# Optimization experiments

Measured on AMD Instinct MI355X. Metric: run time of the kernel, lower is better.

The kernel has to match this reference:

```python
import jax, jax.numpy as jnp
import numpy as np

B, S, D, R, N = 4, 2048, 1024, 256, 16

def setup_inputs() -> dict:
    key = jax.random.key(0)
    k1, k2, k3, k4, k5 = jax.random.split(key, 5)
    return {
        "x": jax.random.normal(k1, (B, S, D), dtype=jnp.float32),
        "feature_know": jax.random.normal(k2, (N, D, R), dtype=jnp.float32) * 0.02,
        "restore_know": jax.random.normal(k3, (N, R, D), dtype=jnp.float32) * 0.02,
        "feature_know_w": jax.random.uniform(k4, (B, S, N), dtype=jnp.float32),
        "restore_know_w": jax.random.uniform(k5, (B, S, N), dtype=jnp.float32),
    }

def reference(x, feature_know, restore_know, feature_know_w, restore_know_w):
    # Feature stage: weighted mixture over N knowledge neurons, D -> R.
    # Same math as einsum('bsd,ndr->bsnr') then einsum('bsnr,bsn->bsr'),
    # fused so the [B,S,N,R] intermediate is reduced over N on the fly.
    h = jnp.einsum('bsd,ndr,bsn->bsr', x, feature_know, feature_know_w)
    # Restore stage: R -> D, again a weighted mixture over N neurons.
    out = jnp.einsum('bsr,nrd,bsn->bsd', h, restore_know, restore_know_w)
    # Dropout is evaluated deterministically (eval mode): identity.
    return out
```

## Files before the change

kernel.cpp:

```cpp
#include <hip/hip_runtime.h>

typedef unsigned short u16;
typedef unsigned int u32;
typedef __attribute__((ext_vector_type(4))) float f32x4;
typedef __attribute__((ext_vector_type(8))) short bf16x8;
typedef __attribute__((ext_vector_type(4))) unsigned short u16x4;

#define MFMA(a, b, c) __builtin_amdgcn_mfma_f32_16x16x32_bf16((a), (b), (c), 0, 0, 0)

static constexpr int M_TOK = 8192;

__device__ __forceinline__ u16 f2bf(float f) {
  u32 u = __float_as_uint(f);
  return (u16)((u + 0x7FFFu + ((u >> 16) & 1u)) >> 16);
}
__device__ __forceinline__ float bf2f(u16 b) {
  u32 u = ((u32)b) << 16;
  return __uint_as_float(u);
}
__device__ __forceinline__ void gload16(const u16* g, u16* l) {
  __builtin_amdgcn_global_load_lds(
      (const __attribute__((address_space(1))) u32*)(const void*)g,
      (__attribute__((address_space(3))) u32*)(void*)l, 16, 0, 0);
}

#define PH_BAR()                                       \
  do {                                                 \
    __builtin_amdgcn_s_barrier();                      \
    asm volatile("s_waitcnt lgkmcnt(0)" ::: "memory"); \
  } while (0)
#define PH_END() __builtin_amdgcn_s_barrier()

__global__ void cast_x_kernel(const float* __restrict__ in, u16* __restrict__ out, int total4) {
  for (int i = blockIdx.x * blockDim.x + threadIdx.x; i < total4; i += gridDim.x * blockDim.x) {
    float4 v = ((const float4*)in)[i];
    u16x4 o;
    o[0] = f2bf(v.x); o[1] = f2bf(v.y); o[2] = f2bf(v.z); o[3] = f2bf(v.w);
    ((u16x4*)out)[i] = o;
  }
}

__global__ void tcast_kernel(const float* __restrict__ in, u16* __restrict__ out, int P, int Q) {
  __shared__ float tile[32][33];
  const int z = blockIdx.z;
  const int q0 = blockIdx.x * 32, p0 = blockIdx.y * 32;
  const float* src = in + (size_t)z * P * Q;
  u16* dst = out + (size_t)z * P * Q;
  const int tx = threadIdx.x & 31, ty = threadIdx.x >> 5;
#pragma unroll
  for (int k = 0; k < 4; ++k)
    tile[ty + k * 8][tx] = src[(size_t)(p0 + ty + k * 8) * Q + q0 + tx];
  __syncthreads();
#pragma unroll
  for (int k = 0; k < 4; ++k)
    dst[(size_t)(q0 + ty + k * 8) * P + p0 + tx] = f2bf(tile[tx][ty + k * 8]);
}

__global__ void combine_h(const u16* __restrict__ T, const float* __restrict__ Wf,
                          u16* __restrict__ h) {
  const int m = blockIdx.x * 4 + (threadIdx.x >> 6);
  const int lane = threadIdx.x & 63;
  const u16* rowp = T + (size_t)m * 4096;
  float h0 = 0.f, h1 = 0.f, h2 = 0.f, h3 = 0.f;
#pragma unroll
  for (int n = 0; n < 16; ++n) {
    u16x4 v = *(const u16x4*)&rowp[n * 256 + lane * 4];
    const float wf = Wf[(size_t)m * 16 + n];
    h0 += wf * bf2f(v[0]); h1 += wf * bf2f(v[1]);
    h2 += wf * bf2f(v[2]); h3 += wf * bf2f(v[3]);
  }
  u16x4 o;
  o[0] = f2bf(h0); o[1] = f2bf(h1); o[2] = f2bf(h2); o[3] = f2bf(h3);
  *(u16x4*)&h[(size_t)m * 256 + lane * 4] = o;
}

template <int NT>
__global__ __launch_bounds__(512, 2) void gemm256(
    const u16* __restrict__ A, const u16* __restrict__ Bm, void* __restrict__ OutV,
    const int N, const int K) {
  constexpr int NITER = NT / 2;
  __shared__ u16 lds[65536];

  const int tid = threadIdx.x;
  const int lane = tid & 63;
  const int wid = tid >> 6;
  const int wr = wid >> 2, wc = wid & 3;

  const int L = blockIdx.y * gridDim.x + blockIdx.x;
  const int ordered = (L & 7) * 64 + (L >> 3);
  const int cid = ordered >> 5, win = ordered & 31;
  const int bx = (cid & 3) * 4 + (win & 3);
  const int by = (cid >> 2) * 8 + (win >> 2);
  const int m0 = by * 256, bn0 = bx * 256;

  const int arow = lane & 15;
  const int acol = (lane >> 4) * 16;
  const int sw = (arow & 7) << 4;
  const int lo0 = arow * 128 + (acol ^ sw);
  const int lo1 = arow * 128 + ((64 + acol) ^ sw);

  const u16* Abase = A + (size_t)m0 * K;
  const u16* Bbase = Bm + (size_t)bn0 * K;

  f32x4 acc[8][4];
#pragma unroll
  for (int i = 0; i < 8; ++i)
#pragma unroll
    for (int j = 0; j < 4; ++j) acc[i][j] = (f32x4){0.f, 0.f, 0.f, 0.f};

  auto STAGE = [&](int b, int isB, int hf, int kt) {
    const u16* G = isB ? Bbase : Abase;
    u16* Lp = &lds[isB * 32768 + (b * 2 + hf) * 8192];
#pragma unroll
    for (int j = 0; j < 2; ++j) {
      const int q = j * 8192 + tid * 16;
      const int grow = q >> 7;
      const int gcol = ((q & 127) ^ (((q >> 7) & 7) << 4)) >> 1;
      gload16(G + (size_t)(hf * 128 + grow) * K + kt * 64 + gcol,
              Lp + ((j * 8192 + wid * 1024) >> 1));
    }
  };
  auto LOAD_AV = [&](bf16x8 (&v)[4][2], int b, int mh) {
    const char* p = (const char*)lds + b * 32768 + (wr * 128 + mh * 64) * 128;
#pragma unroll
    for (int mi = 0; mi < 4; ++mi) {
      v[mi][0] = *(const bf16x8*)(p + mi * 2048 + lo0);
      v[mi][1] = *(const bf16x8*)(p + mi * 2048 + lo1);
    }
  };
  auto LOAD_BV = [&](bf16x8 (&v)[2][2], int b, int nq) {
#pragma unroll
    for (int nj = 0; nj < 2; ++nj) {
      const int rb = wc * 64 + (nq * 2 + nj) * 16;
      const char* p = (const char*)lds + 65536 + b * 32768 + rb * 128;
      v[nj][0] = *(const bf16x8*)(p + lo0);
      v[nj][1] = *(const bf16x8*)(p + lo1);
    }
  };

#define QUAD2(AV, BV0, BV1, MH)                                                \
  do {                                                                         \
    _Pragma("unroll") for (int ks = 0; ks < 2; ++ks) {                         \
      _Pragma("unroll") for (int mi = 0; mi < 4; ++mi) {                       \
        _Pragma("unroll") for (int nj = 0; nj < 2; ++nj) {                     \
          acc[(MH)*4 + mi][nj] = MFMA(AV[mi][ks], BV0[nj][ks], acc[(MH)*4 + mi][nj]); \
          acc[(MH)*4 + mi][2 + nj] = MFMA(AV[mi][ks], BV1[nj][ks], acc[(MH)*4 + mi][2 + nj]); \
        }                                                                      \
      }                                                                        \
    }                                                                          \
  } while (0)

  bf16x8 av[4][2], avh[4][2], bv0[2][2], bv1[2][2];

  STAGE(0, 0, 0, 0); STAGE(0, 0, 1, 0); STAGE(0, 1, 0, 0); STAGE(0, 1, 1, 0);
  STAGE(1, 1, 0, 1); STAGE(1, 0, 0, 1);
  asm volatile("s_waitcnt vmcnt(4)" ::: "memory");
  __builtin_amdgcn_s_barrier();

#pragma unroll 1
  for (int i = 0; i < NITER; ++i) {
    const int ta = 2 * i, tb = ta + 1;
    const bool st = (i + 1 < NITER);
    LOAD_AV(av, 0, 0); LOAD_BV(bv0, 0, 0); LOAD_BV(bv1, 0, 1);
    STAGE(1, 0, 1, tb); STAGE(1, 1, 1, tb);
    PH_BAR();
    __builtin_amdgcn_s_setprio(1);
    QUAD2(av, bv0, bv1, 0);
    __builtin_amdgcn_s_setprio(0);
    PH_END();
    LOAD_AV(avh, 0, 1);
    if (st) { STAGE(0, 1, 0, ta + 2); STAGE(0, 0, 0, ta + 2); }
    PH_BAR();
    __builtin_amdgcn_s_setprio(1);
    QUAD2(avh, bv0, bv1, 1);
    __builtin_amdgcn_s_setprio(0);
    if (st) asm volatile("s_waitcnt vmcnt(4)" ::: "memory");
    else    asm volatile("s_waitcnt vmcnt(0)" ::: "memory");
    PH_END();
    LOAD_AV(av, 1, 0); LOAD_BV(bv0, 1, 0); LOAD_BV(bv1, 1, 1);
    if (st) { STAGE(0, 0, 1, ta + 2); STAGE(0, 1, 1, ta + 2); }
    PH_BAR();
    __builtin_amdgcn_s_setprio(1);
    QUAD2(av, bv0, bv1, 0);
    __builtin_amdgcn_s_setprio(0);
    PH_END();
    LOAD_AV(avh, 1, 1);
    if (st) { STAGE(1, 1, 0, tb + 2); STAGE(1, 0, 0, tb + 2); }
    PH_BAR();
    __builtin_amdgcn_s_setprio(1);
    QUAD2(avh, bv0, bv1, 1);
    __builtin_amdgcn_s_setprio(0);
    if (st) asm volatile("s_waitcnt vmcnt(4)" ::: "memory");
    PH_END();
  }

#pragma unroll
  for (int MI = 0; MI < 8; ++MI) {
    const int r0 = wr * 128 + MI * 16 + (lane >> 4) * 4;
#pragma unroll
    for (int NJ = 0; NJ < 4; ++NJ) {
      const int c = wc * 64 + NJ * 16 + (lane & 15);
#pragma unroll
      for (int j = 0; j < 4; ++j) {
        const int rr = r0 + j;
        *(u16*)((char*)lds + ((rr * 512 + c * 2) ^ ((rr & 7) << 4))) = f2bf(acc[MI][NJ][j]);
      }
    }
  }
  __syncthreads();
#pragma unroll
  for (int i = 0; i < 16; ++i) {
    const int rr = wid * 32 + i * 2 + (lane >> 5);
    const int unit = lane & 31;
    bf16x8 v = *(const bf16x8*)((const char*)lds + ((rr * 512 + unit * 16) ^ ((rr & 7) << 4)));
    *(bf16x8*)((u16*)OutV + (size_t)(m0 + rr) * N + bn0 + unit * 8) = v;
  }
}
#undef QUAD2

__global__ __launch_bounds__(512, 2) void gemm_fold(
    const u16* __restrict__ A,
    const u16* __restrict__ Bn,
    const float* __restrict__ W,
    float* __restrict__ Out) {
  __shared__ u16 ldsB[8][8192];
  __shared__ u16 Wlds[16][264];

  const int tid = threadIdx.x;
  const int lane = tid & 63;
  const int wid = tid >> 6;
  const int kh = wid >> 2;
  const int wrM = (wid >> 1) & 1;
  const int wcN = wid & 1;

  const int L = blockIdx.y * gridDim.x + blockIdx.x;
  const int ordered = (L & 7) * 64 + (L >> 3);
  const int cid = ordered >> 5, win = ordered & 31;
  const int bx = (cid & 3) * 2 + (win & 1);
  const int by = (cid >> 2) * 16 + (win >> 1);
  const int m0 = by * 128, d0 = bx * 128;

  const int arow = lane & 15;
  const int acol = (lane >> 4) * 16;
  const int sw = (arow & 7) << 4;
  const int lo0 = arow * 128 + (acol ^ sw);
  const int lo1 = arow * 128 + ((64 + acol) ^ sw);

  for (int i = tid; i < 128 * 16; i += 512) {
    const int row = i >> 4, n = i & 15;
    Wlds[n][row] = f2bf(W[(size_t)(m0 + row) * 16 + n]);
  }

  auto ASTAGE = [&](int kt) {
    const u16* G = A + (size_t)m0 * 256;
    u16* Lp = &ldsB[kt][0];
#pragma unroll
    for (int j = 0; j < 2; ++j) {
      const int q = j * 8192 + tid * 16;
      const int grow = q >> 7;
      const int gcol = ((q & 127) ^ (((q >> 7) & 7) << 4)) >> 1;
      gload16(G + (size_t)grow * 256 + kt * 64 + gcol, Lp + ((j * 8192 + wid * 1024) >> 1));
    }
  };
  ASTAGE(0); ASTAGE(1); ASTAGE(2); ASTAGE(3);
  __syncthreads();
  bf16x8 avk[4][4];
#pragma unroll
  for (int c2 = 0; c2 < 2; ++c2) {
#pragma unroll
    for (int mi = 0; mi < 4; ++mi) {
      const char* p = (const char*)&ldsB[kh * 2 + c2][0] + (wrM * 64 + mi * 16) * 128;
      avk[c2 * 2 + 0][mi] = *(const bf16x8*)(p + lo0);
      avk[c2 * 2 + 1][mi] = *(const bf16x8*)(p + lo1);
    }
  }
  __syncthreads();

  auto BSTAGE = [&](int ss) {
    const int n = ss >> 1, h = ss & 1, p = ss & 3;
    const u16* G = Bn + ((size_t)n * 1024 + d0) * 256;
#pragma unroll
    for (int t = 0; t < 2; ++t) {
      u16* Lp = &ldsB[2 * p + t][0];
      const int kt = h + 2 * t;
#pragma unroll
      for (int j = 0; j < 2; ++j) {
        const int q = j * 8192 + tid * 16;
        const int grow = q >> 7;
        const int gcol = ((q & 127) ^ (((q >> 7) & 7) << 4)) >> 1;
        gload16(G + (size_t)grow * 256 + kt * 64 + gcol, Lp + ((j * 8192 + wid * 1024) >> 1));
      }
    }
  };

  f32x4 acc_t[4][4], acc_g[4][4];
#pragma unroll
  for (int mi = 0; mi < 4; ++mi)
#pragma unroll
    for (int nj = 0; nj < 4; ++nj) {
      acc_t[mi][nj] = (f32x4){0.f, 0.f, 0.f, 0.f};
      acc_g[mi][nj] = (f32x4){0.f, 0.f, 0.f, 0.f};
    }
  bf16x8 bv[4][2];

  BSTAGE(0); BSTAGE(1); BSTAGE(2);
  asm volatile("s_waitcnt vmcnt(8)" ::: "memory");
  __builtin_amdgcn_s_barrier();

  auto SSTEP = [&](int ss, int h, bool do_stage, int vmsel) {
    const int p = ss & 3;
    const char* pB = (const char*)&ldsB[2 * p + kh][0];
#pragma unroll
    for (int nj = 0; nj < 4; ++nj) {
      const char* q = pB + (wcN * 64 + nj * 16) * 128;
      bv[nj][0] = *(const bf16x8*)(q + lo0);
      bv[nj][1] = *(const bf16x8*)(q + lo1);
    }
    if (do_stage) BSTAGE(ss + 3);
    PH_BAR();
    __builtin_amdgcn_s_setprio(1);
#pragma unroll
    for (int ks = 0; ks < 2; ++ks)
#pragma unroll
      for (int mi = 0; mi < 4; ++mi)
#pragma unroll
        for (int nj = 0; nj < 4; ++nj)
          acc_g[mi][nj] = MFMA(avk[2 * h + ks][mi], bv[nj][ks], acc_g[mi][nj]);
    __builtin_amdgcn_s_setprio(0);
    if (vmsel == 8)      asm volatile("s_waitcnt vmcnt(8)" ::: "memory");
    else if (vmsel == 4) asm volatile("s_waitcnt vmcnt(4)" ::: "memory");
    else if (vmsel == 0) asm volatile("s_waitcnt vmcnt(0)" ::: "memory");
    PH_END();
  };
  auto FOLD = [&](int n) {
#pragma unroll
    for (int mi = 0; mi < 4; ++mi) {
      const int rbase = wrM * 64 + mi * 16 + (lane >> 4) * 4;
      u16x4 wq = *(const u16x4*)&Wlds[n][rbase];
      const float w0 = bf2f(wq[0]), w1 = bf2f(wq[1]), w2 = bf2f(wq[2]), w3 = bf2f(wq[3]);
#pragma unroll
      for (int nj = 0; nj < 4; ++nj) {
        acc_t[mi][nj][0] += w0 * acc_g[mi][nj][0];
        acc_t[mi][nj][1] += w1 * acc_g[mi][nj][1];
        acc_t[mi][nj][2] += w2 * acc_g[mi][nj][2];
        acc_t[mi][nj][3] += w3 * acc_g[mi][nj][3];
        acc_g[mi][nj] = (f32x4){0.f, 0.f, 0.f, 0.f};
      }
    }
  };

#pragma unroll 1
  for (int nn = 0; nn < 14; ++nn) {
    SSTEP(nn * 2 + 0, 0, true, 8);
    SSTEP(nn * 2 + 1, 1, true, 8);
    FOLD(nn);
  }
  SSTEP(28, 0, true, 8);
  SSTEP(29, 1, false, 4);
  FOLD(14);
  SSTEP(30, 0, false, 0);
  SSTEP(31, 1, false, -1);
  FOLD(15);

  __syncthreads();
  float* red = (float*)&ldsB[0][0];
  const int reg = (wrM * 2 + wcN) * 4096;
  if (kh == 1) {
#pragma unroll
    for (int mi = 0; mi < 4; ++mi)
#pragma unroll
      for (int j = 0; j < 4; ++j) {
        const int r = mi * 16 + (lane >> 4) * 4 + j;
#pragma unroll
        for (int nj = 0; nj < 4; ++nj)
          red[reg + r * 64 + nj * 16 + (lane & 15)] = acc_t[mi][nj][j];
      }
  }
  __syncthreads();
  if (kh == 0) {
#pragma unroll
    for (int mi = 0; mi < 4; ++mi) {
      const int rr = mi * 16 + (lane >> 4) * 4;
#pragma unroll
      for (int j = 0; j < 4; ++j) {
        float* orow = Out + (size_t)(m0 + wrM * 64 + rr + j) * 1024 + d0 + wcN * 64 + (lane & 15);
#pragma unroll
        for (int nj = 0; nj < 4; ++nj)
          orow[nj * 16] = acc_t[mi][nj][j] + red[reg + (rr + j) * 64 + nj * 16 + (lane & 15)];
      }
    }
  }
}

extern "C" void kernel_launch(void* const* d_in, const int* in_sizes, int n_in,
                              void* d_out, int out_size, void* d_ws, size_t ws_size,
                              hipStream_t stream) {
  const float* x  = (const float*)d_in[0];
  const float* F  = (const float*)d_in[1];
  const float* Rk = (const float*)d_in[2];
  const float* Wf = (const float*)d_in[3];
  const float* Wr = (const float*)d_in[4];
  float* out = (float*)d_out;

  char* ws = (char*)d_ws;
  u16* X16 = (u16*)(ws);
  u16* B1  = (u16*)(ws + (16u << 20));
  u16* Rt  = (u16*)(ws + (24u << 20));
  u16* T   = (u16*)(ws + (32u << 20));
  u16* h16 = (u16*)(ws);

  cast_x_kernel<<<2048, 256, 0, stream>>>(x, X16, (M_TOK * 1024) / 4);
  tcast_kernel<<<dim3(8, 32, 16), 256, 0, stream>>>(F, B1, 1024, 256);
  tcast_kernel<<<dim3(32, 8, 16), 256, 0, stream>>>(Rk, Rt, 256, 1024);

  gemm256<16><<<dim3(16, 32, 1), 512, 0, stream>>>(X16, B1, T, 4096, 1024);
  combine_h<<<2048, 256, 0, stream>>>(T, Wf, h16);
  gemm_fold<<<dim3(8, 64, 1), 512, 0, stream>>>(h16, Rt, Wr, out);
}
```

Measured before the change: 169.6 us.

## Fuse feature-weight combine into first GEMM epilogue, dropping T intermediate

```diff
diff --git a/kernel.cpp b/kernel.cpp
--- a/kernel.cpp
+++ b/kernel.cpp
@@ -56,30 +56,12 @@
     dst[(size_t)(q0 + ty + k * 8) * P + p0 + tx] = f2bf(tile[tx][ty + k * 8]);
 }
 
-__global__ void combine_h(const u16* __restrict__ T, const float* __restrict__ Wf,
-                          u16* __restrict__ h) {
-  const int m = blockIdx.x * 4 + (threadIdx.x >> 6);
-  const int lane = threadIdx.x & 63;
-  const u16* rowp = T + (size_t)m * 4096;
-  float h0 = 0.f, h1 = 0.f, h2 = 0.f, h3 = 0.f;
-#pragma unroll
-  for (int n = 0; n < 16; ++n) {
-    u16x4 v = *(const u16x4*)&rowp[n * 256 + lane * 4];
-    const float wf = Wf[(size_t)m * 16 + n];
-    h0 += wf * bf2f(v[0]); h1 += wf * bf2f(v[1]);
-    h2 += wf * bf2f(v[2]); h3 += wf * bf2f(v[3]);
-  }
-  u16x4 o;
-  o[0] = f2bf(h0); o[1] = f2bf(h1); o[2] = f2bf(h2); o[3] = f2bf(h3);
-  *(u16x4*)&h[(size_t)m * 256 + lane * 4] = o;
-}
-
-template <int NT>
-__global__ __launch_bounds__(512, 2) void gemm256(
-    const u16* __restrict__ A, const u16* __restrict__ Bm, void* __restrict__ OutV,
-    const int N, const int K) {
-  constexpr int NITER = NT / 2;
+__global__ __launch_bounds__(512, 2) void gemm_h(
+    const u16* __restrict__ A, const u16* __restrict__ Bm,
+    const float* __restrict__ Wf, u16* __restrict__ Hout, const int K) {
+  constexpr int NITER = 8;
   __shared__ u16 lds[65536];
+  __shared__ float wf_lds[256 * 16];
 
   const int tid = threadIdx.x;
   const int lane = tid & 63;
@@ -91,7 +73,7 @@
   const int cid = ordered >> 5, win = ordered & 31;
   const int bx = (cid & 3) * 4 + (win & 3);
   const int by = (cid >> 2) * 8 + (win >> 2);
-  const int m0 = by * 256, bn0 = bx * 256;
+  const int m0 = by * 256, bx16 = bx * 16;
 
   const int arow = lane & 15;
   const int acol = (lane >> 4) * 16;
@@ -100,7 +82,12 @@
   const int lo1 = arow * 128 + ((64 + acol) ^ sw);
 
   const u16* Abase = A + (size_t)m0 * K;
-  const u16* Bbase = Bm + (size_t)bn0 * K;
+
+#pragma unroll
+  for (int t = 0; t < 2; ++t) {
+    const int i4 = t * 512 + tid;
+    *(float4*)&wf_lds[i4 * 4] = *(const float4*)&Wf[(size_t)m0 * 16 + i4 * 4];
+  }
 
   f32x4 acc[8][4];
 #pragma unroll
@@ -109,15 +96,16 @@
     for (int j = 0; j < 4; ++j) acc[i][j] = (f32x4){0.f, 0.f, 0.f, 0.f};
 
   auto STAGE = [&](int b, int isB, int hf, int kt) {
-    const u16* G = isB ? Bbase : Abase;
     u16* Lp = &lds[isB * 32768 + (b * 2 + hf) * 8192];
 #pragma unroll
     for (int j = 0; j < 2; ++j) {
       const int q = j * 8192 + tid * 16;
-      const int grow = q >> 7;
+      const int tr = hf * 128 + (q >> 7);
       const int gcol = ((q & 127) ^ (((q >> 7) & 7) << 4)) >> 1;
-      gload16(G + (size_t)(hf * 128 + grow) * K + kt * 64 + gcol,
-              Lp + ((j * 8192 + wid * 1024) >> 1));
+      const u16* gp = isB
+          ? Bm + (size_t)((tr >> 4) * 256 + bx16 + (tr & 15)) * K + kt * 64 + gcol
+          : Abase + (size_t)tr * K + kt * 64 + gcol;
+      gload16(gp, Lp + ((j * 8192 + wid * 1024) >> 1));
     }
   };
   auto LOAD_AV = [&](bf16x8 (&v)[4][2], int b, int mh) {
@@ -194,26 +182,36 @@
     PH_END();
   }
 
+  __syncthreads();
+  float* pbuf = (float*)lds;
 #pragma unroll
   for (int MI = 0; MI < 8; ++MI) {
-    const int r0 = wr * 128 + MI * 16 + (lane >> 4) * 4;
-#pragma unroll
-    for (int NJ = 0; NJ < 4; ++NJ) {
-      const int c = wc * 64 + NJ * 16 + (lane & 15);
-#pragma unroll
-      for (int j = 0; j < 4; ++j) {
-        const int rr = r0 + j;
-        *(u16*)((char*)lds + ((rr * 512 + c * 2) ^ ((rr & 7) << 4))) = f2bf(acc[MI][NJ][j]);
-      }
-    }
-  }
-  __syncthreads();
-#pragma unroll
-  for (int i = 0; i < 16; ++i) {
-    const int rr = wid * 32 + i * 2 + (lane >> 5);
-    const int unit = lane & 31;
-    bf16x8 v = *(const bf16x8*)((const char*)lds + ((rr * 512 + unit * 16) ^ ((rr & 7) << 4)));
-    *(bf16x8*)((u16*)OutV + (size_t)(m0 + rr) * N + bn0 + unit * 8) = v;
+    const int mbase = wr * 128 + MI * 16 + (lane >> 4) * 4;
+#pragma unroll
+    for (int j = 0; j < 4; ++j) {
+      const float4 wf4 = *(const float4*)&wf_lds[(mbase + j) * 16 + wc * 4];
+      const float p = wf4.x * acc[MI][0][j] + wf4.y * acc[MI][1][j] +
+                      wf4.z * acc[MI][2][j] + wf4.w * acc[MI][3][j];
+      pbuf[wc * 4096 + (mbase + j) * 16 + (lane & 15)] = p;
+    }
+  }
+  __syncthreads();
+  {
+    const int m = tid >> 1, r8 = (tid & 1) * 8;
+    float s[8];
+#pragma unroll
+    for (int r = 0; r < 8; ++r) s[r] = 0.f;
+#pragma unroll
+    for (int w = 0; w < 4; ++w) {
+      const float4 a = *(const float4*)&pbuf[w * 4096 + m * 16 + r8];
+      const float4 b = *(const float4*)&pbuf[w * 4096 + m * 16 + r8 + 4];
+      s[0] += a.x; s[1] += a.y; s[2] += a.z; s[3] += a.w;
+      s[4] += b.x; s[5] += b.y; s[6] += b.z; s[7] += b.w;
+    }
+    bf16x8 o;
+#pragma unroll
+    for (int r = 0; r < 8; ++r) o[r] = (short)f2bf(s[r]);
+    *(bf16x8*)&Hout[(size_t)(m0 + m) * 256 + bx16 + r8] = o;
   }
 }
 #undef QUAD2
@@ -406,14 +404,13 @@
   u16* X16 = (u16*)(ws);
   u16* B1  = (u16*)(ws + (16u << 20));
   u16* Rt  = (u16*)(ws + (24u << 20));
-  u16* T   = (u16*)(ws + (32u << 20));
-  u16* h16 = (u16*)(ws);
+  u16* h16 = (u16*)(ws + (32u << 20));
 
   cast_x_kernel<<<2048, 256, 0, stream>>>(x, X16, (M_TOK * 1024) / 4);
   tcast_kernel<<<dim3(8, 32, 16), 256, 0, stream>>>(F, B1, 1024, 256);
   tcast_kernel<<<dim3(32, 8, 16), 256, 0, stream>>>(Rk, Rt, 256, 1024);
 
-  gemm256<16><<<dim3(16, 32, 1), 512, 0, stream>>>(X16, B1, T, 4096, 1024);
-  combine_h<<<2048, 256, 0, stream>>>(T, Wf, h16);
+  gemm_h<<<dim3(16, 32, 1), 512, 0, stream>>>(X16, B1, Wf, h16, 1024);
+
   gemm_fold<<<dim3(8, 64, 1), 512, 0, stream>>>(h16, Rt, Wr, out);
 }
```

New measurement: 149.8 us. 1.13x faster.
